# Performance work log

Measured on AMD Instinct MI355X. Metric: run time of the kernel, lower is better.

Reference implementation:

```python
import jax, jax.numpy as jnp
import numpy as np

SEQ, DM, STATE, BATCH = 1024, 512, 16, 8
D2 = 2 * DM
EPS = 1e-5


def rmsnorm(x, w):
    return x * jax.lax.rsqrt(jnp.mean(x * x, axis=-1, keepdims=True) + EPS) * w


def setup_inputs() -> dict:
    key = jax.random.key(0)
    ks = jax.random.split(key, 16)
    def lin(k, i, o):
        k1, k2 = jax.random.split(k)
        s = 1.0 / np.sqrt(i)
        return (jax.random.uniform(k1, (i, o), minval=-s, maxval=s),
                jax.random.uniform(k2, (o,), minval=-s, maxval=s))
    inp_w, inp_b = lin(ks[0], DM, D2)
    convlin_w, convlin_b = lin(ks[1], D2, D2)
    fc1_w, fc1_b = lin(ks[2], D2, D2)
    fc2_w, fc2_b = lin(ks[3], D2, STATE)
    fc3_w, fc3_b = lin(ks[4], D2, STATE)
    D_w, D_b = lin(ks[5], DM, D2)
    out_w, _ = lin(ks[6], D2, DM)
    out_b = jnp.ones((DM,))  # nn.init.constant_(out_proj.bias, 1.0)
    # Conv1d(seq_len, seq_len, k=3): weight (out_ch=SEQ, in_ch=SEQ, 3)
    s = 1.0 / np.sqrt(SEQ * 3)
    conv_w = jax.random.uniform(ks[7], (SEQ, SEQ, 3), minval=-s, maxval=s)
    conv_b = jax.random.uniform(ks[8], (SEQ,), minval=-s, maxval=s)
    norm_w = jnp.ones((DM,))
    x = jax.random.normal(ks[9], (BATCH, SEQ, DM))
    return dict(x=x, norm_w=norm_w, inp_w=inp_w, inp_b=inp_b, conv_w=conv_w,
                conv_b=conv_b, convlin_w=convlin_w, convlin_b=convlin_b,
                fc1_w=fc1_w, fc1_b=fc1_b, fc2_w=fc2_w, fc2_b=fc2_b,
                fc3_w=fc3_w, fc3_b=fc3_b, D_w=D_w, D_b=D_b,
                out_w=out_w, out_b=out_b)


def reference(x, norm_w, inp_w, inp_b, conv_w, conv_b, convlin_w, convlin_b,
              fc1_w, fc1_b, fc2_w, fc2_b, fc3_w, fc3_b, D_w, D_b, out_w, out_b):
    xn = rmsnorm(x, norm_w)                                  # (b, L, d)
    x_proj = xn @ inp_w + inp_b                              # (b, L, 2d)
    # Conv1d over channels=seq_len, spatial=2d, padding=1
    x_conv = jax.lax.conv_general_dilated(
        x_proj, conv_w, window_strides=(1,), padding=[(1, 1)],
        dimension_numbers=('NCH', 'OIH', 'NCH')) + conv_b[None, :, None]
    x_conv_out = jax.nn.silu(x_conv) @ convlin_w + convlin_b  # (b, L, 2d)
    # S6: h starts at zero so dA term vanishes; y = x*delta*sum_n(B*C)
    u = x_conv_out
    B = u @ fc2_w + fc2_b                                     # (b, L, n)
    C = u @ fc3_w + fc3_b                                     # (b, L, n)
    delta = jax.nn.softplus(u @ fc1_w + fc1_b)                # (b, L, 2d)
    bc = jnp.sum(B * C, axis=-1, keepdims=True)               # (b, L, 1)
    x_ssm = u * delta * bc                                    # (b, L, 2d)
    x_act = jax.nn.silu(x_ssm)
    x_residual = jax.nn.silu(xn @ D_w + D_b)
    return (x_residual * x_act) @ out_w + out_b               # (b, L, d)
```

## Files before the change

### kernel.cpp

```cpp
#include <hip/hip_runtime.h>
#include <hip/hip_bf16.h>

#define SEQ 1024
#define DM 512
#define D2 1024
#define NSTATE 16
#define BATCH 8
#define ROWS (BATCH * SEQ)
#define EPSF 1e-5f

typedef __attribute__((ext_vector_type(8))) short bf16x8;
typedef __attribute__((ext_vector_type(4))) float f32x4;

#define AS1 __attribute__((address_space(1)))
#define AS3 __attribute__((address_space(3)))

__device__ __forceinline__ void gll16(const void* g, void* l) {
    __builtin_amdgcn_global_load_lds(
        (const AS1 unsigned int*)(uintptr_t)g,
        (AS3 unsigned int*)(unsigned int)(uintptr_t)l, 16, 0, 0);
}

__device__ __forceinline__ float sigmoidf_(float x) {
    return 1.f / (1.f + __expf(-x));
}
__device__ __forceinline__ unsigned short f2bf(float f) {
    __hip_bfloat16 h = __float2bfloat16(f);
    unsigned short r;
    __builtin_memcpy(&r, &h, 2);
    return r;
}

__global__ __launch_bounds__(256) void prep_all(
    const float* s0, const float* s1, const float* s2, const float* s3,
    const float* s4, const float* s5, const float* s6,
    __hip_bfloat16* d0, __hip_bfloat16* d1, __hip_bfloat16* d2,
    __hip_bfloat16* d3, __hip_bfloat16* d4, __hip_bfloat16* d5,
    __hip_bfloat16* d6) {
    const int j = blockIdx.z;
    int R, C;
    const float* src;
    __hip_bfloat16* dst;
    switch (j) {
        case 0: src = s0; dst = d0; R = 512; C = 1024; break;
        case 1: src = s1; dst = d1; R = 512; C = 1024; break;
        case 2: src = s2; dst = d2; R = 1024; C = 1024; break;
        case 3: src = s3; dst = d3; R = 1024; C = 1024; break;
        case 4: src = s4; dst = d4; R = 1024; C = 512; break;
        case 5: src = s5; dst = d5; R = 1024; C = 16; break;
        default: src = s6; dst = d6; R = 1024; C = 16; break;
    }
    int c0 = blockIdx.x * 32, r0 = blockIdx.y * 32;
    if (c0 >= C || r0 >= R) return;
    __shared__ float tile[32][33];
    int tx = threadIdx.x & 31, ty = threadIdx.x >> 5;
#pragma unroll
    for (int p = 0; p < 4; ++p) {
        int r = r0 + ty + p * 8, c = c0 + tx;
        if (r < R && c < C) tile[ty + p * 8][tx] = src[(size_t)r * C + c];
    }
    __syncthreads();
#pragma unroll
    for (int p = 0; p < 4; ++p) {
        int c = c0 + ty + p * 8, r = r0 + tx;
        if (r < R && c < C)
            dst[(size_t)c * R + r] = __float2bfloat16(tile[tx][ty + p * 8]);
    }
}

__global__ __launch_bounds__(256) void convw_k(const float* __restrict__ cw,
                                               __hip_bfloat16* __restrict__ wk) {
    int idx = blockIdx.x * 256 + threadIdx.x;
    float a = cw[(size_t)idx * 3 + 0];
    float b = cw[(size_t)idx * 3 + 1];
    float c = cw[(size_t)idx * 3 + 2];
    wk[idx] = __float2bfloat16(a);
    wk[(size_t)SEQ * SEQ + idx] = __float2bfloat16(b);
    wk[(size_t)2 * SEQ * SEQ + idx] = __float2bfloat16(c);
}

__global__ __launch_bounds__(256) void rmsnorm_k(
    const float* __restrict__ x, const float* __restrict__ w,
    __hip_bfloat16* __restrict__ o) {
    int row = blockIdx.x;
    const float* xr = x + (size_t)row * DM;
    __hip_bfloat16* orow = o + (size_t)row * DM;
    int t = threadIdx.x;
    float v0 = xr[t];
    float v1 = xr[t + 256];
    float ss = v0 * v0 + v1 * v1;
#pragma unroll
    for (int off = 32; off; off >>= 1) ss += __shfl_down(ss, off, 64);
    __shared__ float parts[4];
    if ((t & 63) == 0) parts[t >> 6] = ss;
    __syncthreads();
    float tot = parts[0] + parts[1] + parts[2] + parts[3];
    float rs = rsqrtf(tot * (1.f / DM) + EPSF);
    orow[t] = __float2bfloat16(v0 * rs * w[t]);
    orow[t + 256] = __float2bfloat16(v1 * rs * w[t + 256]);
}

template <int EPI, int KC>
__global__ __launch_bounds__(256) void mgemm(
    const __hip_bfloat16* __restrict__ A, const __hip_bfloat16* __restrict__ Bt,
    const float* __restrict__ bias, void* __restrict__ outp,
    void* __restrict__ outp2, const float* __restrict__ bias2,
    const __hip_bfloat16* __restrict__ uptr,
    const __hip_bfloat16* __restrict__ resid, const float* __restrict__ bcv,
    int M, int N) {
    __shared__ __align__(16) __hip_bfloat16 As[4][128 * 32];
    __shared__ __align__(16) __hip_bfloat16 Bs[4][128 * 32];
    const int nbx = gridDim.x;
    int lin = blockIdx.y * nbx + blockIdx.x;
    int chunk = (nbx * gridDim.y) >> 3;
    int wg = (lin & 7) * chunk + (lin >> 3);
    const int n0 = (wg % nbx) * 128, m0 = (wg / nbx) * 128;
    const int t = threadIdx.x, lane = t & 63, w = t >> 6;
    const int wr = w >> 1, wc = w & 1;
    const int l15 = lane & 15, l4 = lane >> 4;

    const int r0_ = t >> 2, c0_ = (t & 3) ^ ((r0_ >> 1) & 3);
    const int b1 = 256 + t, r1_ = b1 >> 2, c1_ = (b1 & 3) ^ ((r1_ >> 1) & 3);
    const __hip_bfloat16* gA0 = A + (size_t)(m0 + r0_) * KC + c0_ * 8;
    const __hip_bfloat16* gA1 = A + (size_t)(m0 + r1_) * KC + c1_ * 8;
    const __hip_bfloat16* gB0 = Bt + (size_t)(n0 + r0_) * KC + c0_ * 8;
    const __hip_bfloat16* gB1 = Bt + (size_t)(n0 + r1_) * KC + c1_ * 8;
    const int d0 = (w * 64) * 8, d1 = (256 + w * 64) * 8;

    int offA[4], offB[4];
#pragma unroll
    for (int i = 0; i < 4; ++i) {
        int ra = wr * 64 + i * 16 + l15;
        offA[i] = (ra * 4 + (l4 ^ ((ra >> 1) & 3))) * 8;
        int rb = wc * 64 + i * 16 + l15;
        offB[i] = (rb * 4 + (l4 ^ ((rb >> 1) & 3))) * 8;
    }

#define MSTAGE(BUF, K0)                  \
    {                                    \
        gll16(gA0 + (K0), &As[BUF][d0]); \
        gll16(gA1 + (K0), &As[BUF][d1]); \
        gll16(gB0 + (K0), &Bs[BUF][d0]); \
        gll16(gB1 + (K0), &Bs[BUF][d1]); \
    }

    f32x4 acc[4][4] = {};
    constexpr int NT = KC >> 6;
    MSTAGE(0, 0);
    MSTAGE(1, 32);
    asm volatile("s_waitcnt vmcnt(0)" ::: "memory");
    __builtin_amdgcn_s_barrier();
    __builtin_amdgcn_sched_barrier(0);

#pragma unroll 1
    for (int p = 0; p < NT; ++p) {
        const int kA = 2 * p, kB = 2 * p + 1;
        const int bufA = kA & 3, bufB = kB & 3;
        if (p + 1 < NT) {
            MSTAGE((kA + 2) & 3, (kA + 2) * 32);
            MSTAGE((kB + 2) & 3, (kB + 2) * 32);
        }
        bf16x8 a0[4], b0[4], a1[4], b1v[4];
#pragma unroll
        for (int i = 0; i < 4; ++i) {
            a0[i] = *(const bf16x8*)&As[bufA][offA[i]];
            b0[i] = *(const bf16x8*)&Bs[bufA][offB[i]];
        }
#pragma unroll
        for (int i = 0; i < 4; ++i) {
            a1[i] = *(const bf16x8*)&As[bufB][offA[i]];
            b1v[i] = *(const bf16x8*)&Bs[bufB][offB[i]];
        }
        __builtin_amdgcn_s_setprio(1);
#pragma unroll
        for (int i = 0; i < 4; ++i)
#pragma unroll
            for (int j = 0; j < 4; ++j)
                acc[i][j] = __builtin_amdgcn_mfma_f32_16x16x32_bf16(
                    a0[i], b0[j], acc[i][j], 0, 0, 0);
#pragma unroll
        for (int i = 0; i < 4; ++i)
#pragma unroll
            for (int j = 0; j < 4; ++j)
                acc[i][j] = __builtin_amdgcn_mfma_f32_16x16x32_bf16(
                    a1[i], b1v[j], acc[i][j], 0, 0, 0);
        __builtin_amdgcn_s_setprio(0);
        if (p + 1 < NT) {
            asm volatile("s_waitcnt vmcnt(0)" ::: "memory");
            __builtin_amdgcn_s_barrier();
            __builtin_amdgcn_sched_barrier(0);
        }
    }
#undef MSTAGE

    const int mb = m0 + wr * 64, nb = n0 + wc * 64;
#pragma unroll
    for (int i = 0; i < 4; ++i) {
#pragma unroll
        for (int j = 0; j < 4; ++j) {
            int ngl = nb + j * 16 + l15;
            if (EPI == 5) {
                if (nb < D2) {
                    float bj = bias[ngl];
                    int b = m0 >> 10;
                    int ibase = (mb & (SEQ - 1)) + i * 16 + l4 * 4;
                    ushort4 pk;
                    pk.x = f2bf(acc[i][j][0] + bj);
                    pk.y = f2bf(acc[i][j][1] + bj);
                    pk.z = f2bf(acc[i][j][2] + bj);
                    pk.w = f2bf(acc[i][j][3] + bj);
                    *(ushort4*)((__hip_bfloat16*)outp +
                                ((size_t)b * D2 + ngl) * SEQ + ibase) = pk;
                } else {
                    int ng2 = ngl - D2;
                    float bj = bias2[ng2];
#pragma unroll
                    for (int r = 0; r < 4; ++r) {
                        int mg = mb + i * 16 + l4 * 4 + r;
                        float c = acc[i][j][r] + bj;
                        ((__hip_bfloat16*)outp2)[(size_t)mg * D2 + ng2] =
                            __float2bfloat16(c * sigmoidf_(c));
                    }
                }
            } else {
                float bj = bias[ngl];
#pragma unroll
                for (int r = 0; r < 4; ++r) {
                    int mg = mb + i * 16 + l4 * 4 + r;
                    size_t ro = (size_t)mg * N + ngl;
                    float c = acc[i][j][r] + bj;
                    if (EPI == 1) {
                        ((__hip_bfloat16*)outp)[ro] = __float2bfloat16(c);
                    } else if (EPI == 3) {
                        float sp = (c > 20.f) ? c : log1pf(__expf(c));
                        float xs = __bfloat162float(uptr[ro]) * sp * bcv[mg];
                        float v = __bfloat162float(resid[ro]) *
                                  (xs * sigmoidf_(xs));
                        ((__hip_bfloat16*)outp)[ro] = __float2bfloat16(v);
                    } else {
                        ((float*)outp)[ro] = c;
                    }
                }
            }
        }
    }
}

__global__ __launch_bounds__(256) void conv_mfma(
    const __hip_bfloat16* __restrict__ wk,
    const __hip_bfloat16* __restrict__ Xt,
    const float* __restrict__ cb, __hip_bfloat16* __restrict__ outp) {
    __shared__ __align__(16) __hip_bfloat16 Ws[2][3][128 * 32];
    __shared__ __align__(16) __hip_bfloat16 Xs[2][128 * 32];
    __shared__ __align__(16) __hip_bfloat16 Xh[2][SEQ];
    int lin = blockIdx.x + 8 * blockIdx.y + 64 * blockIdx.z;
    int wg = (lin & 7) * 64 + (lin >> 3);
    const int n0 = (wg & 7) * 128;
    const int m0 = ((wg >> 3) & 7) * 128;
    const int z = wg >> 6;
    const int t = threadIdx.x, lane = t & 63, w = t >> 6;
    const int wr = w >> 1, wc = w & 1;
    const int l15 = lane & 15, l4 = lane >> 4;
    const __hip_bfloat16* Xtb = Xt + (size_t)z * D2 * SEQ;

    {
        int which = t >> 7;
        int col = (t & 127) * 8;
        int h = n0 - 1 + which * 129;
        uint4 v = make_uint4(0u, 0u, 0u, 0u);
        if (h >= 0 && h < D2)
            v = *(const uint4*)(Xtb + (size_t)h * SEQ + col);
        *(uint4*)&Xh[which][col] = v;
    }

    int rowp[2], cbw[2];
#pragma unroll
    for (int p = 0; p < 2; ++p) {
        int blk = p * 256 + t;
        rowp[p] = blk >> 2;
        cbw[p] = (blk & 3) ^ ((rowp[p] >> 1) & 3);
    }
    const __hip_bfloat16* wsrc[2][3];
    const __hip_bfloat16* xsrc[2];
#pragma unroll
    for (int p = 0; p < 2; ++p) {
#pragma unroll
        for (int tp = 0; tp < 3; ++tp)
            wsrc[p][tp] = wk + (size_t)tp * SEQ * SEQ +
                          (size_t)(m0 + rowp[p]) * SEQ + cbw[p] * 8;
        xsrc[p] = Xtb + (size_t)(n0 + rowp[p]) * SEQ + cbw[p] * 8;
    }
    const int dst0 = (w * 64) * 8, dst1 = (256 + w * 64) * 8;

    int offA[4];
#pragma unroll
    for (int i = 0; i < 4; ++i) {
        int ra = wr * 64 + i * 16 + l15;
        offA[i] = (ra * 4 + (l4 ^ ((ra >> 1) & 3))) * 8;
    }

#define CSTAGE(BUF, K0)                              \
    {                                                \
        gll16(wsrc[0][0] + (K0), &Ws[BUF][0][dst0]); \
        gll16(wsrc[1][0] + (K0), &Ws[BUF][0][dst1]); \
        gll16(wsrc[0][1] + (K0), &Ws[BUF][1][dst0]); \
        gll16(wsrc[1][1] + (K0), &Ws[BUF][1][dst1]); \
        gll16(wsrc[0][2] + (K0), &Ws[BUF][2][dst0]); \
        gll16(wsrc[1][2] + (K0), &Ws[BUF][2][dst1]); \
        gll16(xsrc[0] + (K0), &Xs[BUF][dst0]);       \
        gll16(xsrc[1] + (K0), &Xs[BUF][dst1]);       \
    }

    f32x4 acc[4][4] = {};
    CSTAGE(0, 0);
    asm volatile("s_waitcnt lgkmcnt(0)" ::: "memory");

#pragma unroll 1
    for (int kt = 0; kt < 32; ++kt) {
        const int k0 = kt * 32;
        const int buf = kt & 1;
        if (kt + 1 < 32) {
            CSTAGE(buf ^ 1, (kt + 1) * 32);
            asm volatile("s_waitcnt vmcnt(8)" ::: "memory");
        } else {
            asm volatile("s_waitcnt vmcnt(0)" ::: "memory");
        }
        __builtin_amdgcn_s_barrier();
        __builtin_amdgcn_sched_barrier(0);
        bf16x8 aw[3][4];
#pragma unroll
        for (int tp = 0; tp < 3; ++tp)
#pragma unroll
            for (int i = 0; i < 4; ++i)
                aw[tp][i] = *(const bf16x8*)&Ws[buf][tp][offA[i]];
        __builtin_amdgcn_s_setprio(1);
#pragma unroll
        for (int j = 0; j < 4; ++j) {
#pragma unroll
            for (int tp = 0; tp < 3; ++tp) {
                int rb = wc * 64 + j * 16 + l15 + tp;
                int r = rb - 1;
                const __hip_bfloat16* src =
                    &Xs[buf][(r * 4 + (l4 ^ ((r >> 1) & 3))) * 8];
                if (rb == 0) src = &Xh[0][k0 + l4 * 8];
                if (rb == 129) src = &Xh[1][k0 + l4 * 8];
                bf16x8 bvx = *(const bf16x8*)src;
#pragma unroll
                for (int i = 0; i < 4; ++i)
                    acc[i][j] = __builtin_amdgcn_mfma_f32_16x16x32_bf16(
                        aw[tp][i], bvx, acc[i][j], 0, 0, 0);
            }
        }
        __builtin_amdgcn_s_setprio(0);
        if (kt + 1 < 32) {
            __builtin_amdgcn_s_barrier();
            __builtin_amdgcn_sched_barrier(0);
        }
    }
#undef CSTAGE

    const int mb = m0 + wr * 64, nb = n0 + wc * 64;
    size_t ob = (size_t)z * SEQ * D2;
#pragma unroll
    for (int i = 0; i < 4; ++i)
#pragma unroll
        for (int j = 0; j < 4; ++j)
#pragma unroll
            for (int r = 0; r < 4; ++r) {
                int mg = mb + i * 16 + l4 * 4 + r;
                int ng = nb + j * 16 + l15;
                float c = acc[i][j][r] + cb[mg];
                outp[ob + (size_t)mg * D2 + ng] =
                    __float2bfloat16(c * sigmoidf_(c));
            }
}

__global__ __launch_bounds__(256) void bc2_k(
    const __hip_bfloat16* __restrict__ u, const __hip_bfloat16* __restrict__ fcT,
    const float* __restrict__ b2, const float* __restrict__ b3,
    float* __restrict__ bc) {
    __shared__ __align__(16) __hip_bfloat16 Bl[32 * 1024];
    __shared__ __align__(16) __hip_bfloat16 As[3][128 * 32];
    const int m0 = blockIdx.x * 128;
    const int t = threadIdx.x, lane = t & 63, w = t >> 6;
    const int l15 = lane & 15, l4 = lane >> 4;

#pragma unroll
    for (int it = 0; it < 16; ++it) {
        int q = it * 256 + t;
        int n = q >> 7, blk = q & 127;
        uint4 v = *(const uint4*)(fcT + (size_t)n * 1024 + blk * 8);
        *(uint4*)&Bl[(n * 128 + (blk ^ (n & 7))) * 8] = v;
    }

    const int r0_ = t >> 2, c0_ = (t & 3) ^ ((r0_ >> 1) & 3);
    const int bq = 256 + t, r1_ = bq >> 2, c1_ = (bq & 3) ^ ((r1_ >> 1) & 3);
    const __hip_bfloat16* gA0 = u + (size_t)(m0 + r0_) * 1024 + c0_ * 8;
    const __hip_bfloat16* gA1 = u + (size_t)(m0 + r1_) * 1024 + c1_ * 8;
    const int d0 = (w * 64) * 8, d1 = (256 + w * 64) * 8;

    int offA[2];
#pragma unroll
    for (int i = 0; i < 2; ++i) {
        int ra = w * 32 + i * 16 + l15;
        offA[i] = (ra * 4 + (l4 ^ ((ra >> 1) & 3))) * 8;
    }

#define BSTAGE(BUF, K0)                  \
    {                                    \
        gll16(gA0 + (K0), &As[BUF][d0]); \
        gll16(gA1 + (K0), &As[BUF][d1]); \
    }

    f32x4 acc[2][2] = {};
    unsigned curb = 0, nxtb = 1, thdb = 2;
    BSTAGE(0, 0);
    BSTAGE(1, 32);
    asm volatile("s_waitcnt vmcnt(2)" ::: "memory");
    __builtin_amdgcn_s_barrier();
    __builtin_amdgcn_sched_barrier(0);

#pragma unroll 1
    for (int kt = 0; kt < 32; ++kt) {
        const bool st = (kt + 2 < 32);
        if (st) BSTAGE(thdb, (kt + 2) * 32);
        bf16x8 af[2], bf[2];
#pragma unroll
        for (int i = 0; i < 2; ++i) af[i] = *(const bf16x8*)&As[curb][offA[i]];
#pragma unroll
        for (int nj = 0; nj < 2; ++nj) {
            int n = nj * 16 + l15;
            int blk = (kt * 4 + l4) ^ (n & 7);
            bf[nj] = *(const bf16x8*)&Bl[(n * 128 + blk) * 8];
        }
#pragma unroll
        for (int i = 0; i < 2; ++i)
#pragma unroll
            for (int nj = 0; nj < 2; ++nj)
                acc[i][nj] = __builtin_amdgcn_mfma_f32_16x16x32_bf16(
                    af[i], bf[nj], acc[i][nj], 0, 0, 0);
        if (kt + 1 < 32) {
            if (st)
                asm volatile("s_waitcnt vmcnt(2)" ::: "memory");
            else
                asm volatile("s_waitcnt vmcnt(0)" ::: "memory");
            __builtin_amdgcn_s_barrier();
            __builtin_amdgcn_sched_barrier(0);
        }
        unsigned tb = curb;
        curb = nxtb;
        nxtb = thdb;
        thdb = tb;
    }
#undef BSTAGE

    float bb2 = b2[l15], bb3 = b3[l15];
#pragma unroll
    for (int i = 0; i < 2; ++i)
#pragma unroll
        for (int r = 0; r < 4; ++r) {
            float Bv = acc[i][0][r] + bb2;
            float Cv = acc[i][1][r] + bb3;
            float p = Bv * Cv;
            p += __shfl_xor(p, 1, 64);
            p += __shfl_xor(p, 2, 64);
            p += __shfl_xor(p, 4, 64);
            p += __shfl_xor(p, 8, 64);
            if (l15 == 0)
                bc[m0 + w * 32 + i * 16 + l4 * 4 + r] = p;
        }
}

extern "C" void kernel_launch(void* const* d_in, const int* in_sizes, int n_in,
                              void* d_out, int out_size, void* d_ws,
                              size_t ws_size, hipStream_t stream) {
    const float* x = (const float*)d_in[0];
    const float* norm_w = (const float*)d_in[1];
    const float* inp_w = (const float*)d_in[2];
    const float* inp_b = (const float*)d_in[3];
    const float* conv_w = (const float*)d_in[4];
    const float* conv_b = (const float*)d_in[5];
    const float* convlin_w = (const float*)d_in[6];
    const float* convlin_b = (const float*)d_in[7];
    const float* fc1_w = (const float*)d_in[8];
    const float* fc1_b = (const float*)d_in[9];
    const float* fc2_w = (const float*)d_in[10];
    const float* fc2_b = (const float*)d_in[11];
    const float* fc3_w = (const float*)d_in[12];
    const float* fc3_b = (const float*)d_in[13];
    const float* D_w = (const float*)d_in[14];
    const float* D_b = (const float*)d_in[15];
    const float* out_w = (const float*)d_in[16];
    const float* out_b = (const float*)d_in[17];
    float* out = (float*)d_out;

    __hip_bfloat16* xnb = (__hip_bfloat16*)d_ws;
    __hip_bfloat16* xt = xnb + (size_t)ROWS * DM;
    __hip_bfloat16* cvo = xt + (size_t)BATCH * D2 * SEQ;
    __hip_bfloat16* u = cvo + (size_t)ROWS * D2;
    __hip_bfloat16* resid = u + (size_t)ROWS * D2;
    __hip_bfloat16* Wcat = resid + (size_t)ROWS * D2;
    __hip_bfloat16* clT = Wcat + (size_t)2 * D2 * DM;
    __hip_bfloat16* fc1T = clT + (size_t)D2 * D2;
    __hip_bfloat16* outT = fc1T + (size_t)D2 * D2;
    __hip_bfloat16* wk = outT + (size_t)DM * D2;
    __hip_bfloat16* fcT = wk + (size_t)3 * SEQ * SEQ;
    float* bcb = (float*)(fcT + (size_t)32 * D2);

    prep_all<<<dim3(32, 32, 7), 256, 0, stream>>>(
        inp_w, D_w, convlin_w, fc1_w, out_w, fc2_w, fc3_w, Wcat,
        Wcat + (size_t)D2 * DM, clT, fc1T, outT, fcT, fcT + (size_t)16 * D2);
    convw_k<<<SEQ * SEQ / 256, 256, 0, stream>>>(conv_w, wk);
    rmsnorm_k<<<ROWS, 256, 0, stream>>>(x, norm_w, xnb);
    mgemm<5, DM><<<dim3(2 * D2 / 128, ROWS / 128), 256, 0, stream>>>(
        xnb, Wcat, inp_b, xt, resid, D_b, nullptr, nullptr, nullptr, ROWS,
        2 * D2);
    conv_mfma<<<dim3(D2 / 128, SEQ / 128, BATCH), 256, 0, stream>>>(
        wk, xt, conv_b, cvo);
    mgemm<1, D2><<<dim3(D2 / 128, ROWS / 128), 256, 0, stream>>>(
        cvo, clT, convlin_b, u, nullptr, nullptr, nullptr, nullptr, nullptr,
        ROWS, D2);
    bc2_k<<<ROWS / 128, 256, 0, stream>>>(u, fcT, fc2_b, fc3_b, bcb);
    mgemm<3, D2><<<dim3(D2 / 128, ROWS / 128), 256, 0, stream>>>(
        u, fc1T, fc1_b, cvo, nullptr, nullptr, u, resid, bcb, ROWS, D2);
    mgemm<4, D2><<<dim3(DM / 128, ROWS / 128), 256, 0, stream>>>(
        cvo, outT, out_b, out, nullptr, nullptr, nullptr, nullptr, nullptr,
        ROWS, DM);
}
```

Before: 224.4 us.

## Enlarge GEMM tiles to 256x128 with 8 waves and a triple-buffered K=64 pipeline

```diff
diff --git a/kernel.cpp b/kernel.cpp
--- a/kernel.cpp
+++ b/kernel.cpp
@@ -101,97 +101,133 @@
 }
 
 template <int EPI, int KC>
-__global__ __launch_bounds__(256) void mgemm(
+__global__ __launch_bounds__(512) void mgemm(
     const __hip_bfloat16* __restrict__ A, const __hip_bfloat16* __restrict__ Bt,
     const float* __restrict__ bias, void* __restrict__ outp,
     void* __restrict__ outp2, const float* __restrict__ bias2,
     const __hip_bfloat16* __restrict__ uptr,
     const __hip_bfloat16* __restrict__ resid, const float* __restrict__ bcv,
     int M, int N) {
-    __shared__ __align__(16) __hip_bfloat16 As[4][128 * 32];
-    __shared__ __align__(16) __hip_bfloat16 Bs[4][128 * 32];
+    __shared__ __align__(16) __hip_bfloat16 As[3][256 * 64];
+    __shared__ __align__(16) __hip_bfloat16 Bs[3][128 * 64];
     const int nbx = gridDim.x;
     int lin = blockIdx.y * nbx + blockIdx.x;
     int chunk = (nbx * gridDim.y) >> 3;
     int wg = (lin & 7) * chunk + (lin >> 3);
-    const int n0 = (wg % nbx) * 128, m0 = (wg / nbx) * 128;
+    const int n0 = (wg % nbx) * 128, m0 = (wg / nbx) * 256;
     const int t = threadIdx.x, lane = t & 63, w = t >> 6;
     const int wr = w >> 1, wc = w & 1;
     const int l15 = lane & 15, l4 = lane >> 4;
 
-    const int r0_ = t >> 2, c0_ = (t & 3) ^ ((r0_ >> 1) & 3);
-    const int b1 = 256 + t, r1_ = b1 >> 2, c1_ = (b1 & 3) ^ ((r1_ >> 1) & 3);
-    const __hip_bfloat16* gA0 = A + (size_t)(m0 + r0_) * KC + c0_ * 8;
-    const __hip_bfloat16* gA1 = A + (size_t)(m0 + r1_) * KC + c1_ * 8;
-    const __hip_bfloat16* gB0 = Bt + (size_t)(n0 + r0_) * KC + c0_ * 8;
-    const __hip_bfloat16* gB1 = Bt + (size_t)(n0 + r1_) * KC + c1_ * 8;
-    const int d0 = (w * 64) * 8, d1 = (256 + w * 64) * 8;
-
-    int offA[4], offB[4];
+    const __hip_bfloat16* srcA[4];
+    const __hip_bfloat16* srcB[2];
+    int dA[4], dB[2];
+#pragma unroll
+    for (int p = 0; p < 4; ++p) {
+        int q = p * 512 + t, r = q >> 3, cs = (q & 7) ^ (r & 7);
+        srcA[p] = A + (size_t)(m0 + r) * KC + cs * 8;
+        dA[p] = q * 8;
+    }
+#pragma unroll
+    for (int p = 0; p < 2; ++p) {
+        int q = p * 512 + t, r = q >> 3, cs = (q & 7) ^ (r & 7);
+        srcB[p] = Bt + (size_t)(n0 + r) * KC + cs * 8;
+        dB[p] = q * 8;
+    }
+
+    int offA[4][2], offB[4][2];
 #pragma unroll
     for (int i = 0; i < 4; ++i) {
         int ra = wr * 64 + i * 16 + l15;
-        offA[i] = (ra * 4 + (l4 ^ ((ra >> 1) & 3))) * 8;
         int rb = wc * 64 + i * 16 + l15;
-        offB[i] = (rb * 4 + (l4 ^ ((rb >> 1) & 3))) * 8;
-    }
-
-#define MSTAGE(BUF, K0)                  \
-    {                                    \
-        gll16(gA0 + (K0), &As[BUF][d0]); \
-        gll16(gA1 + (K0), &As[BUF][d1]); \
-        gll16(gB0 + (K0), &Bs[BUF][d0]); \
-        gll16(gB1 + (K0), &Bs[BUF][d1]); \
+#pragma unroll
+        for (int h = 0; h < 2; ++h) {
+            offA[i][h] = (ra * 8 + ((h * 4 + l4) ^ (ra & 7))) * 8;
+            offB[i][h] = (rb * 8 + ((h * 4 + l4) ^ (rb & 7))) * 8;
+        }
+    }
+
+#define SGH0(BUF, K0)                         \
+    {                                         \
+        gll16(srcA[0] + (K0), &As[BUF][dA[0]]); \
+        gll16(srcA[1] + (K0), &As[BUF][dA[1]]); \
+        gll16(srcB[0] + (K0), &Bs[BUF][dB[0]]); \
+    }
+#define SGH1(BUF, K0)                         \
+    {                                         \
+        gll16(srcA[2] + (K0), &As[BUF][dA[2]]); \
+        gll16(srcA[3] + (K0), &As[BUF][dA[3]]); \
+        gll16(srcB[1] + (K0), &Bs[BUF][dB[1]]); \
     }
 
     f32x4 acc[4][4] = {};
     constexpr int NT = KC >> 6;
-    MSTAGE(0, 0);
-    MSTAGE(1, 32);
-    asm volatile("s_waitcnt vmcnt(0)" ::: "memory");
+    int b0 = 0, b1 = 1, b2 = 2;
+    SGH0(0, 0);
+    SGH1(0, 0);
+    SGH0(1, 64);
+    SGH1(1, 64);
+    asm volatile("s_waitcnt vmcnt(6)" ::: "memory");
     __builtin_amdgcn_s_barrier();
     __builtin_amdgcn_sched_barrier(0);
 
 #pragma unroll 1
-    for (int p = 0; p < NT; ++p) {
-        const int kA = 2 * p, kB = 2 * p + 1;
-        const int bufA = kA & 3, bufB = kB & 3;
-        if (p + 1 < NT) {
-            MSTAGE((kA + 2) & 3, (kA + 2) * 32);
-            MSTAGE((kB + 2) & 3, (kB + 2) * 32);
-        }
-        bf16x8 a0[4], b0[4], a1[4], b1v[4];
+    for (int kt = 0; kt < NT; ++kt) {
+        const bool st = (kt + 2 < NT);
+        bf16x8 a0[4], v0[4];
 #pragma unroll
         for (int i = 0; i < 4; ++i) {
-            a0[i] = *(const bf16x8*)&As[bufA][offA[i]];
-            b0[i] = *(const bf16x8*)&Bs[bufA][offB[i]];
-        }
-#pragma unroll
-        for (int i = 0; i < 4; ++i) {
-            a1[i] = *(const bf16x8*)&As[bufB][offA[i]];
-            b1v[i] = *(const bf16x8*)&Bs[bufB][offB[i]];
-        }
+            a0[i] = *(const bf16x8*)&As[b0][offA[i][0]];
+            v0[i] = *(const bf16x8*)&Bs[b0][offB[i][0]];
+        }
+        if (st) SGH0(b2, (kt + 2) * 64);
+        __builtin_amdgcn_sched_barrier(0);
+        __builtin_amdgcn_s_barrier();
+        asm volatile("s_waitcnt lgkmcnt(0)" ::: "memory");
+        __builtin_amdgcn_sched_barrier(0);
         __builtin_amdgcn_s_setprio(1);
 #pragma unroll
         for (int i = 0; i < 4; ++i)
 #pragma unroll
             for (int j = 0; j < 4; ++j)
                 acc[i][j] = __builtin_amdgcn_mfma_f32_16x16x32_bf16(
-                    a0[i], b0[j], acc[i][j], 0, 0, 0);
+                    a0[i], v0[j], acc[i][j], 0, 0, 0);
+        __builtin_amdgcn_s_setprio(0);
+        __builtin_amdgcn_s_barrier();
+        bf16x8 a1[4], v1[4];
+#pragma unroll
+        for (int i = 0; i < 4; ++i) {
+            a1[i] = *(const bf16x8*)&As[b0][offA[i][1]];
+            v1[i] = *(const bf16x8*)&Bs[b0][offB[i][1]];
+        }
+        if (st) SGH1(b2, (kt + 2) * 64);
+        __builtin_amdgcn_sched_barrier(0);
+        __builtin_amdgcn_s_barrier();
+        asm volatile("s_waitcnt lgkmcnt(0)" ::: "memory");
+        __builtin_amdgcn_sched_barrier(0);
+        __builtin_amdgcn_s_setprio(1);
 #pragma unroll
         for (int i = 0; i < 4; ++i)
 #pragma unroll
             for (int j = 0; j < 4; ++j)
                 acc[i][j] = __builtin_amdgcn_mfma_f32_16x16x32_bf16(
-                    a1[i], b1v[j], acc[i][j], 0, 0, 0);
+                    a1[i], v1[j], acc[i][j], 0, 0, 0);
         __builtin_amdgcn_s_setprio(0);
-        if (p + 1 < NT) {
-            asm volatile("s_waitcnt vmcnt(0)" ::: "memory");
+        if (kt + 1 < NT) {
+            if (st)
+                asm volatile("s_waitcnt vmcnt(6)" ::: "memory");
+            else
+                asm volatile("s_waitcnt vmcnt(0)" ::: "memory");
             __builtin_amdgcn_s_barrier();
             __builtin_amdgcn_sched_barrier(0);
         }
-    }
-#undef MSTAGE
+        int tb = b0;
+        b0 = b1;
+        b1 = b2;
+        b2 = tb;
+    }
+#undef SGH0
+#undef SGH1
 
     const int mb = m0 + wr * 64, nb = n0 + wc * 64;
 #pragma unroll
@@ -512,18 +548,18 @@
         Wcat + (size_t)D2 * DM, clT, fc1T, outT, fcT, fcT + (size_t)16 * D2);
     convw_k<<<SEQ * SEQ / 256, 256, 0, stream>>>(conv_w, wk);
     rmsnorm_k<<<ROWS, 256, 0, stream>>>(x, norm_w, xnb);
-    mgemm<5, DM><<<dim3(2 * D2 / 128, ROWS / 128), 256, 0, stream>>>(
+    mgemm<5, DM><<<dim3(2 * D2 / 128, ROWS / 256), 512, 0, stream>>>(
         xnb, Wcat, inp_b, xt, resid, D_b, nullptr, nullptr, nullptr, ROWS,
         2 * D2);
     conv_mfma<<<dim3(D2 / 128, SEQ / 128, BATCH), 256, 0, stream>>>(
         wk, xt, conv_b, cvo);
-    mgemm<1, D2><<<dim3(D2 / 128, ROWS / 128), 256, 0, stream>>>(
+    mgemm<1, D2><<<dim3(D2 / 128, ROWS / 256), 512, 0, stream>>>(
         cvo, clT, convlin_b, u, nullptr, nullptr, nullptr, nullptr, nullptr,
         ROWS, D2);
     bc2_k<<<ROWS / 128, 256, 0, stream>>>(u, fcT, fc2_b, fc3_b, bcb);
-    mgemm<3, D2><<<dim3(D2 / 128, ROWS / 128), 256, 0, stream>>>(
+    mgemm<3, D2><<<dim3(D2 / 128, ROWS / 256), 512, 0, stream>>>(
         u, fc1T, fc1_b, cvo, nullptr, nullptr, u, resid, bcb, ROWS, D2);
-    mgemm<4, D2><<<dim3(DM / 128, ROWS / 128), 256, 0, stream>>>(
+    mgemm<4, D2><<<dim3(DM / 128, ROWS / 256), 512, 0, stream>>>(
         cvo, outT, out_b, out, nullptr, nullptr, nullptr, nullptr, nullptr,
         ROWS, DM);
 }
```

New measurement: 227.7 us. About the same (+1.4%).

## Switch GEMM to 32x32x16 MFMA with triple-buffered single-tile pipeline

Applied to the files above, without the earlier changes.

```diff
diff --git a/kernel.cpp b/kernel.cpp
--- a/kernel.cpp
+++ b/kernel.cpp
@@ -11,6 +11,7 @@
 
 typedef __attribute__((ext_vector_type(8))) short bf16x8;
 typedef __attribute__((ext_vector_type(4))) float f32x4;
+typedef __attribute__((ext_vector_type(16))) float f32x16;
 
 #define AS1 __attribute__((address_space(1)))
 #define AS3 __attribute__((address_space(3)))
@@ -100,6 +101,10 @@
     orow[t + 256] = __float2bfloat16(v1 * rs * w[t + 256]);
 }
 
+__device__ __forceinline__ int lkey(int r) {
+    return ((r >> 1) & 1) | (((r >> 3) & 1) << 1);
+}
+
 template <int EPI, int KC>
 __global__ __launch_bounds__(256) void mgemm(
     const __hip_bfloat16* __restrict__ A, const __hip_bfloat16* __restrict__ Bt,
@@ -108,8 +113,8 @@
     const __hip_bfloat16* __restrict__ uptr,
     const __hip_bfloat16* __restrict__ resid, const float* __restrict__ bcv,
     int M, int N) {
-    __shared__ __align__(16) __hip_bfloat16 As[4][128 * 32];
-    __shared__ __align__(16) __hip_bfloat16 Bs[4][128 * 32];
+    __shared__ __align__(16) __hip_bfloat16 As[3][128 * 32];
+    __shared__ __align__(16) __hip_bfloat16 Bs[3][128 * 32];
     const int nbx = gridDim.x;
     int lin = blockIdx.y * nbx + blockIdx.x;
     int chunk = (nbx * gridDim.y) >> 3;
@@ -117,23 +122,26 @@
     const int n0 = (wg % nbx) * 128, m0 = (wg / nbx) * 128;
     const int t = threadIdx.x, lane = t & 63, w = t >> 6;
     const int wr = w >> 1, wc = w & 1;
-    const int l15 = lane & 15, l4 = lane >> 4;
-
-    const int r0_ = t >> 2, c0_ = (t & 3) ^ ((r0_ >> 1) & 3);
-    const int b1 = 256 + t, r1_ = b1 >> 2, c1_ = (b1 & 3) ^ ((r1_ >> 1) & 3);
+    const int lc = lane & 31, h2 = lane >> 5;
+
+    const int q0 = t, r0_ = q0 >> 2, c0_ = (q0 & 3) ^ lkey(r0_);
+    const int q1 = 256 + t, r1_ = q1 >> 2, c1_ = (q1 & 3) ^ lkey(r1_);
     const __hip_bfloat16* gA0 = A + (size_t)(m0 + r0_) * KC + c0_ * 8;
     const __hip_bfloat16* gA1 = A + (size_t)(m0 + r1_) * KC + c1_ * 8;
     const __hip_bfloat16* gB0 = Bt + (size_t)(n0 + r0_) * KC + c0_ * 8;
     const __hip_bfloat16* gB1 = Bt + (size_t)(n0 + r1_) * KC + c1_ * 8;
     const int d0 = (w * 64) * 8, d1 = (256 + w * 64) * 8;
 
-    int offA[4], offB[4];
-#pragma unroll
-    for (int i = 0; i < 4; ++i) {
-        int ra = wr * 64 + i * 16 + l15;
-        offA[i] = (ra * 4 + (l4 ^ ((ra >> 1) & 3))) * 8;
-        int rb = wc * 64 + i * 16 + l15;
-        offB[i] = (rb * 4 + (l4 ^ ((rb >> 1) & 3))) * 8;
+    int offA[2][2], offB[2][2];
+#pragma unroll
+    for (int ti = 0; ti < 2; ++ti) {
+        int ra = wr * 64 + ti * 32 + lc;
+        int rb = wc * 64 + ti * 32 + lc;
+#pragma unroll
+        for (int kk = 0; kk < 2; ++kk) {
+            offA[ti][kk] = (ra * 4 + ((2 * kk + h2) ^ lkey(ra))) * 8;
+            offB[ti][kk] = (rb * 4 + ((2 * kk + h2) ^ lkey(rb))) * 8;
+        }
     }
 
 #define MSTAGE(BUF, K0)                  \
@@ -144,80 +152,82 @@
         gll16(gB1 + (K0), &Bs[BUF][d1]); \
     }
 
-    f32x4 acc[4][4] = {};
-    constexpr int NT = KC >> 6;
+    f32x16 acc[2][2] = {};
+    constexpr int NT = KC >> 5;
+    unsigned curb = 0, nxtb = 1, thdb = 2;
     MSTAGE(0, 0);
     MSTAGE(1, 32);
-    asm volatile("s_waitcnt vmcnt(0)" ::: "memory");
+    asm volatile("s_waitcnt vmcnt(4)" ::: "memory");
     __builtin_amdgcn_s_barrier();
     __builtin_amdgcn_sched_barrier(0);
 
 #pragma unroll 1
-    for (int p = 0; p < NT; ++p) {
-        const int kA = 2 * p, kB = 2 * p + 1;
-        const int bufA = kA & 3, bufB = kB & 3;
-        if (p + 1 < NT) {
-            MSTAGE((kA + 2) & 3, (kA + 2) * 32);
-            MSTAGE((kB + 2) & 3, (kB + 2) * 32);
-        }
-        bf16x8 a0[4], b0[4], a1[4], b1v[4];
-#pragma unroll
-        for (int i = 0; i < 4; ++i) {
-            a0[i] = *(const bf16x8*)&As[bufA][offA[i]];
-            b0[i] = *(const bf16x8*)&Bs[bufA][offB[i]];
-        }
-#pragma unroll
-        for (int i = 0; i < 4; ++i) {
-            a1[i] = *(const bf16x8*)&As[bufB][offA[i]];
-            b1v[i] = *(const bf16x8*)&Bs[bufB][offB[i]];
-        }
+    for (int kt = 0; kt < NT; ++kt) {
+        const bool st = (kt + 2 < NT);
+        if (st) MSTAGE(thdb, (kt + 2) * 32);
+        bf16x8 af[2][2], bv[2][2];
+#pragma unroll
+        for (int kk = 0; kk < 2; ++kk)
+#pragma unroll
+            for (int ti = 0; ti < 2; ++ti) {
+                af[kk][ti] = *(const bf16x8*)&As[curb][offA[ti][kk]];
+                bv[kk][ti] = *(const bf16x8*)&Bs[curb][offB[ti][kk]];
+            }
         __builtin_amdgcn_s_setprio(1);
 #pragma unroll
-        for (int i = 0; i < 4; ++i)
-#pragma unroll
-            for (int j = 0; j < 4; ++j)
-                acc[i][j] = __builtin_amdgcn_mfma_f32_16x16x32_bf16(
-                    a0[i], b0[j], acc[i][j], 0, 0, 0);
-#pragma unroll
-        for (int i = 0; i < 4; ++i)
-#pragma unroll
-            for (int j = 0; j < 4; ++j)
-                acc[i][j] = __builtin_amdgcn_mfma_f32_16x16x32_bf16(
-                    a1[i], b1v[j], acc[i][j], 0, 0, 0);
+        for (int kk = 0; kk < 2; ++kk)
+#pragma unroll
+            for (int ti = 0; ti < 2; ++ti)
+#pragma unroll
+                for (int tj = 0; tj < 2; ++tj)
+                    acc[ti][tj] = __builtin_amdgcn_mfma_f32_32x32x16_bf16(
+                        af[kk][ti], bv[kk][tj], acc[ti][tj], 0, 0, 0);
         __builtin_amdgcn_s_setprio(0);
-        if (p + 1 < NT) {
-            asm volatile("s_waitcnt vmcnt(0)" ::: "memory");
+        if (kt + 1 < NT) {
+            if (st)
+                asm volatile("s_waitcnt vmcnt(4)" ::: "memory");
+            else
+                asm volatile("s_waitcnt vmcnt(0)" ::: "memory");
             __builtin_amdgcn_s_barrier();
             __builtin_amdgcn_sched_barrier(0);
         }
+        unsigned tb = curb;
+        curb = nxtb;
+        nxtb = thdb;
+        thdb = tb;
     }
 #undef MSTAGE
 
     const int mb = m0 + wr * 64, nb = n0 + wc * 64;
 #pragma unroll
-    for (int i = 0; i < 4; ++i) {
-#pragma unroll
-        for (int j = 0; j < 4; ++j) {
-            int ngl = nb + j * 16 + l15;
+    for (int ti = 0; ti < 2; ++ti) {
+#pragma unroll
+        for (int tj = 0; tj < 2; ++tj) {
+            int ngl = nb + tj * 32 + lc;
             if (EPI == 5) {
                 if (nb < D2) {
                     float bj = bias[ngl];
                     int b = m0 >> 10;
-                    int ibase = (mb & (SEQ - 1)) + i * 16 + l4 * 4;
-                    ushort4 pk;
-                    pk.x = f2bf(acc[i][j][0] + bj);
-                    pk.y = f2bf(acc[i][j][1] + bj);
-                    pk.z = f2bf(acc[i][j][2] + bj);
-                    pk.w = f2bf(acc[i][j][3] + bj);
-                    *(ushort4*)((__hip_bfloat16*)outp +
-                                ((size_t)b * D2 + ngl) * SEQ + ibase) = pk;
+                    int ibase = (mb & (SEQ - 1)) + ti * 32 + 4 * h2;
+#pragma unroll
+                    for (int g = 0; g < 4; ++g) {
+                        ushort4 pk;
+                        pk.x = f2bf(acc[ti][tj][4 * g + 0] + bj);
+                        pk.y = f2bf(acc[ti][tj][4 * g + 1] + bj);
+                        pk.z = f2bf(acc[ti][tj][4 * g + 2] + bj);
+                        pk.w = f2bf(acc[ti][tj][4 * g + 3] + bj);
+                        *(ushort4*)((__hip_bfloat16*)outp +
+                                    ((size_t)b * D2 + ngl) * SEQ + ibase +
+                                    8 * g) = pk;
+                    }
                 } else {
                     int ng2 = ngl - D2;
                     float bj = bias2[ng2];
 #pragma unroll
-                    for (int r = 0; r < 4; ++r) {
-                        int mg = mb + i * 16 + l4 * 4 + r;
-                        float c = acc[i][j][r] + bj;
+                    for (int r = 0; r < 16; ++r) {
+                        int mg = mb + ti * 32 + (r & 3) + 8 * (r >> 2) +
+                                 4 * h2;
+                        float c = acc[ti][tj][r] + bj;
                         ((__hip_bfloat16*)outp2)[(size_t)mg * D2 + ng2] =
                             __float2bfloat16(c * sigmoidf_(c));
                     }
@@ -225,10 +235,10 @@
             } else {
                 float bj = bias[ngl];
 #pragma unroll
-                for (int r = 0; r < 4; ++r) {
-                    int mg = mb + i * 16 + l4 * 4 + r;
+                for (int r = 0; r < 16; ++r) {
+                    int mg = mb + ti * 32 + (r & 3) + 8 * (r >> 2) + 4 * h2;
                     size_t ro = (size_t)mg * N + ngl;
-                    float c = acc[i][j][r] + bj;
+                    float c = acc[ti][tj][r] + bj;
                     if (EPI == 1) {
                         ((__hip_bfloat16*)outp)[ro] = __float2bfloat16(c);
                     } else if (EPI == 3) {
```

After: 230.4 us. 2.7% more time.
